# Kernel tuning notes

Hardware: AMD Instinct MI355X
Metric: run time of the kernel (lower is better)

Reference implementation:

```python
import jax, jax.numpy as jnp
import numpy as np

B, T, D, H = 4, 2048, 1024, 16
DK = D // H


def setup_inputs() -> dict:
    key = jax.random.key(0)
    ks = jax.random.split(key, 9)
    s = 1.0 / np.sqrt(D)
    x = jax.random.normal(ks[0], (B, T, D), dtype=jnp.float32)
    mask = jnp.tril(jnp.ones((T, T), dtype=bool))[None, None]  # causal [1,1,T,T]
    wq = jax.random.uniform(ks[1], (D, D), jnp.float32, -s, s)
    bq = jax.random.uniform(ks[2], (D,), jnp.float32, -s, s)
    wk = jax.random.uniform(ks[3], (D, D), jnp.float32, -s, s)
    bk = jax.random.uniform(ks[4], (D,), jnp.float32, -s, s)
    wv = jax.random.uniform(ks[5], (D, D), jnp.float32, -s, s)
    bv = jax.random.uniform(ks[6], (D,), jnp.float32, -s, s)
    wo = jax.random.uniform(ks[7], (D, D), jnp.float32, -s, s)
    bo = jax.random.uniform(ks[8], (D,), jnp.float32, -s, s)
    return {"x": x, "mask": mask, "wq": wq, "bq": bq, "wk": wk, "bk": bk,
            "wv": wv, "bv": bv, "wo": wo, "bo": bo}


def reference(x, mask, wq, bq, wk, bk, wv, bv, wo, bo):
    # projections: torch Linear is x @ W.T + b; here weights stored as (D, D) used directly
    q = (x @ wq + bq).reshape(B, T, H, DK).transpose(0, 2, 1, 3)  # [B,H,T,dk]
    k = (x @ wk + bk).reshape(B, T, H, DK).transpose(0, 2, 1, 3)
    v = (x @ wv + bv).reshape(B, T, H, DK).transpose(0, 2, 1, 3)
    scores = jnp.einsum('bhqd,bhkd->bhqk', q, k) / jnp.sqrt(jnp.float32(DK))
    scores = jnp.where(mask, scores, -jnp.inf)
    attn = jax.nn.softmax(scores, axis=-1)
    # dropout p=0.0 -> identity
    y = jnp.einsum('bhqk,bhkd->bhqd', attn, v)
    y = y.transpose(0, 2, 1, 3).reshape(B, T, D)
    return y @ wo + bo
```

## Files before the change

kernel.cpp:

```cpp
#include <hip/hip_runtime.h>


typedef short s16x8 __attribute__((ext_vector_type(8)));
typedef short s16x4 __attribute__((ext_vector_type(4)));
typedef float f32x4 __attribute__((ext_vector_type(4)));
typedef unsigned int u32x2 __attribute__((ext_vector_type(2)));

static __device__ __forceinline__ float bf2f(unsigned short u) {
    return __uint_as_float(((unsigned int)u) << 16);
}
static __device__ __forceinline__ unsigned short f2bf(float f) {
    unsigned int x = __float_as_uint(f);
    unsigned int r = x + 0x7fffu + ((x >> 16) & 1u);
    return (unsigned short)(r >> 16);
}

static __device__ __forceinline__ void gload_lds16(const short* g, short* l) {
    __builtin_amdgcn_global_load_lds((__attribute__((address_space(1))) void*)g,
                                     (__attribute__((address_space(3))) void*)l, 16, 0, 0);
}

static __device__ __forceinline__ unsigned int cvt_pk_bf16(float a, float b) {
    unsigned int r;
    asm("v_cvt_pk_bf16_f32 %0, %1, %2" : "=v"(r) : "v"(a), "v"(b));
    return r;
}

__global__ __launch_bounds__(64) void detect_dtype(const unsigned short* __restrict__ x,
                                                   int* __restrict__ flag) {
    int lane = threadIdx.x;
    int cnt = 0;
    for (int i = 0; i < 64; ++i) {
        float v = bf2f(x[lane * 64 + i]);
        if (!(fabsf(v) < 1e10f)) cnt++;
    }
    unsigned long long m = __ballot(cnt > 0);
    if (lane == 0) *flag = (m != 0ull) ? 1 : 0;
}

__global__ __launch_bounds__(256) void convert_bf16(const void* __restrict__ src,
                                                    unsigned short* __restrict__ dst,
                                                    int n, const int* __restrict__ flag) {
    int i = blockIdx.x * 256 + threadIdx.x;
    if (i >= n) return;
    if (*flag) dst[i] = f2bf(((const float*)src)[i]);
    else       dst[i] = ((const unsigned short*)src)[i];
}

__global__ __launch_bounds__(256) void convert_biases(const void* __restrict__ b0,
                                                      const void* __restrict__ b1,
                                                      const void* __restrict__ b2,
                                                      const void* __restrict__ b3,
                                                      unsigned short* __restrict__ dst,
                                                      const int* __restrict__ flag) {
    int i = blockIdx.x * 256 + threadIdx.x;
    const void* src = (i < 1024) ? b0 : (i < 2048 ? b1 : (i < 3072 ? b2 : b3));
    int k = i & 1023;
    if (*flag) dst[i] = f2bf(((const float*)src)[k]);
    else       dst[i] = ((const unsigned short*)src)[k];
}

__global__ __launch_bounds__(256) void transpose_wt(const void* __restrict__ src,
                                                    unsigned short* __restrict__ dst,
                                                    const int* __restrict__ flag) {
    __shared__ unsigned short t[32][33];
    int f = *flag;
    int x = threadIdx.x, y = threadIdx.y;
    int n0 = blockIdx.x * 32, k0 = blockIdx.y * 32;
    for (int j = 0; j < 32; j += 8) {
        size_t idx = (size_t)(k0 + y + j) * 1024 + n0 + x;
        t[y + j][x] = f ? f2bf(((const float*)src)[idx]) : ((const unsigned short*)src)[idx];
    }
    __syncthreads();
    for (int j = 0; j < 32; j += 8) dst[(size_t)(n0 + y + j) * 1024 + k0 + x] = t[x][y + j];
}

__global__ __launch_bounds__(256) void gemm_bf16(const short* __restrict__ A,
                                                 const short* __restrict__ Bt,
                                                 void* __restrict__ C,
                                                 short* __restrict__ vt,
                                                 const unsigned short* __restrict__ bq,
                                                 const unsigned short* __restrict__ bk,
                                                 const unsigned short* __restrict__ bv,
                                                 int K, int ldc,
                                                 const int* __restrict__ flag, int f32out,
                                                 int scale_q, int fuse_v) {
    __shared__ __align__(16) short As[128][32];
    __shared__ __align__(16) short Bs[128][32];
    int tid = threadIdx.x;
    int wid = tid >> 6, lane = tid & 63, quad = lane >> 4, l16 = lane & 15;
    int wm = wid & 1, wn = wid >> 1;
    int m0 = blockIdx.x * 128, n0 = blockIdx.y * 128;
    bool wf = f32out && (*flag != 0);

    int lrow = lane >> 2;
    int lcol = (lane & 3) * 8;
    const short* Ag0 = A  + (size_t)(m0 + wid * 32 + lrow) * K + lcol;
    const short* Ag1 = A  + (size_t)(m0 + wid * 32 + 16 + lrow) * K + lcol;
    const short* Bg0 = Bt + (size_t)(n0 + wid * 32 + lrow) * K + lcol;
    const short* Bg1 = Bt + (size_t)(n0 + wid * 32 + 16 + lrow) * K + lcol;
    short* Al0 = &As[wid * 32][0];
    short* Al1 = &As[wid * 32 + 16][0];
    short* Bl0 = &Bs[wid * 32][0];
    short* Bl1 = &Bs[wid * 32 + 16][0];

    f32x4 acc[4][4] = {};
    for (int k0 = 0; k0 < K; k0 += 32) {
        __syncthreads();
        gload_lds16(Ag0 + k0, Al0);
        gload_lds16(Ag1 + k0, Al1);
        gload_lds16(Bg0 + k0, Bl0);
        gload_lds16(Bg1 + k0, Bl1);
        __syncthreads();
        s16x8 a[4], b[4];
        for (int i = 0; i < 4; ++i) a[i] = *(const s16x8*)&As[wm * 64 + i * 16 + l16][quad * 8];
        for (int j = 0; j < 4; ++j) b[j] = *(const s16x8*)&Bs[wn * 64 + j * 16 + l16][quad * 8];
        for (int i = 0; i < 4; ++i)
            for (int j = 0; j < 4; ++j)
                acc[i][j] = __builtin_amdgcn_mfma_f32_16x16x32_bf16(a[i], b[j], acc[i][j], 0, 0, 0);
    }
    for (int j = 0; j < 4; ++j) {
        int col = n0 + wn * 64 + j * 16 + l16;
        const unsigned short* bptr = (col < 1024) ? bq : (col < 2048 ? bk : bv);
        float bias = bf2f(bptr[col & 1023]);
        float cs = (scale_q && col < 1024) ? 0.18033688f : 1.0f;
        for (int i = 0; i < 4; ++i) {
            int rbase = m0 + wm * 64 + i * 16 + quad * 4;
            if (fuse_v && col >= 2048) {
                int h = (col - 2048) >> 6, dk = col & 63;
                int bb_ = rbase >> 11, t = rbase & 2047;
                s16x4 pk;
                for (int r = 0; r < 4; ++r) pk[r] = (short)f2bf(acc[i][j][r] + bias);
                *(s16x4*)(vt + ((size_t)((bb_ * 16 + h) * 64 + dk)) * 2048 + t) = pk;
            } else {
                for (int r = 0; r < 4; ++r) {
                    float v = (acc[i][j][r] + bias) * cs;
                    size_t idx = (size_t)(rbase + r) * ldc + col;
                    if (wf) ((float*)C)[idx] = v;
                    else    ((unsigned short*)C)[idx] = f2bf(v);
                }
            }
        }
    }
}

static __device__ __forceinline__ void stage_tiles(const short* kbase, const short* vbase,
                                                   int kt, short* Kb, short* Vb,
                                                   int wid, int lane) {
    int row = wid * 8 + (lane >> 3);
    int c_src = (lane & 7) ^ (lane >> 3);
    const short* kg = kbase + (size_t)(kt * 64 + row) * 3072 + c_src * 8;
    const short* vg = vbase + (size_t)row * 2048 + kt * 64 + c_src * 8;
    gload_lds16(kg, Kb + wid * 512);
    gload_lds16(vg, Vb + wid * 512);
}

static __device__ __forceinline__ s16x8 lds_frag(const short* buf, int row, int cg) {
    int slot = cg ^ (row & 7);
    return *(const s16x8*)(buf + row * 64 + slot * 8);
}

__global__ __launch_bounds__(512, 4) void attn(const short* __restrict__ qkv,
                                               const short* __restrict__ vt,
                                               unsigned short* __restrict__ y) {
    __shared__ __align__(16) short Kbuf[3][64 * 64];
    __shared__ __align__(16) short Vbuf[3][64 * 64];
    __shared__ __align__(16) short Ps[8][16 * 68];
    int tid = threadIdx.x;
    int wid = tid >> 6, lane = tid & 63, quad = lane >> 4, l16 = lane & 15;
    int bh = blockIdx.x, b = bh >> 4, h = bh & 15;
    const short* kbase = qkv + (size_t)b * 2048 * 3072 + 1024 + h * 64;
    const short* vbase = vt + (size_t)bh * 64 * 2048;
    short* PsW = &Ps[wid][0];

    s16x8 ones;
    for (int e = 0; e < 8; ++e) ones[e] = (short)0x3F80;

    int qb = 15 - (int)blockIdx.y;
    int ktmax = 2 * qb + 1;
    int kmax_w = 2 * qb + (wid >> 2);

    const short* qp = qkv + (size_t)(b * 2048 + qb * 128 + wid * 16 + l16) * 3072 + h * 64;
    s16x8 q0 = *(const s16x8*)(qp + quad * 8);
    s16x8 q1 = *(const s16x8*)(qp + 32 + quad * 8);

    float m_old = -INFINITY;
    f32x4 lacc = {0.f, 0.f, 0.f, 0.f};
    f32x4 o[4] = {};

    stage_tiles(kbase, vbase, 0, &Kbuf[0][0], &Vbuf[0][0], wid, lane);
    stage_tiles(kbase, vbase, 1, &Kbuf[1][0], &Vbuf[1][0], wid, lane);
    int ss = 2;
    int cc = 0;

    for (int kt = 0; kt <= ktmax; ++kt) {
        if (kt < ktmax) asm volatile("s_waitcnt vmcnt(2)" ::: "memory");
        else            asm volatile("s_waitcnt vmcnt(0)" ::: "memory");
        __builtin_amdgcn_sched_barrier(0);
        __builtin_amdgcn_s_barrier();

        if (kt + 2 <= ktmax) {
            stage_tiles(kbase, vbase, kt + 2, &Kbuf[0][0] + ss * 4096, &Vbuf[0][0] + ss * 4096,
                        wid, lane);
            ss = (ss == 2) ? 0 : ss + 1;
        }

        if (kt <= kmax_w) {
            const short* Kb = &Kbuf[0][0] + cc * 4096;
            const short* Vb = &Vbuf[0][0] + cc * 4096;

            f32x4 s[4] = {};
            __builtin_amdgcn_s_setprio(1);
            for (int j = 0; j < 4; ++j) {
                s16x8 klo = lds_frag(Kb, j * 16 + l16, quad);
                s16x8 khi = lds_frag(Kb, j * 16 + l16, 4 + quad);
                s[j] = __builtin_amdgcn_mfma_f32_16x16x32_bf16(klo, q0, s[j], 0, 0, 0);
                s[j] = __builtin_amdgcn_mfma_f32_16x16x32_bf16(khi, q1, s[j], 0, 0, 0);
            }
            __builtin_amdgcn_s_setprio(0);

            if (kt == kmax_w) {
                int qq = (wid & 3) * 16 + l16;
                for (int j = 0; j < 4; ++j)
                    for (int r = 0; r < 4; ++r)
                        if (j * 16 + quad * 4 + r > qq) s[j][r] = -INFINITY;
            }

            float mj0 = fmaxf(fmaxf(s[0][0], s[0][1]), s[0][2]);
            mj0 = fmaxf(mj0, s[0][3]);
            float mj1 = fmaxf(fmaxf(s[1][0], s[1][1]), s[1][2]);
            mj1 = fmaxf(mj1, s[1][3]);
            float mj2 = fmaxf(fmaxf(s[2][0], s[2][1]), s[2][2]);
            mj2 = fmaxf(mj2, s[2][3]);
            float mj3 = fmaxf(fmaxf(s[3][0], s[3][1]), s[3][2]);
            mj3 = fmaxf(mj3, s[3][3]);
            float mx = fmaxf(fmaxf(fmaxf(mj0, mj1), mj2), mj3);
            mx = fmaxf(mx, __shfl_xor(mx, 16));
            mx = fmaxf(mx, __shfl_xor(mx, 32));

            if (__any(mx > m_old + 8.0f)) {
                float mn = fmaxf(m_old, mx);
                float alpha = exp2f(m_old - mn);
                m_old = mn;
                float ar[4];
                for (int r = 0; r < 4; ++r) ar[r] = __shfl(alpha, quad * 4 + r);
                for (int r = 0; r < 4; ++r) {
                    lacc[r] *= ar[r];
                    for (int d = 0; d < 4; ++d) o[d][r] *= ar[r];
                }
            }

            for (int j = 0; j < 4; ++j) {
                float p0 = exp2f(s[j][0] - m_old);
                float p1 = exp2f(s[j][1] - m_old);
                float p2 = exp2f(s[j][2] - m_old);
                float p3 = exp2f(s[j][3] - m_old);
                u32x2 w;
                w.x = cvt_pk_bf16(p0, p1);
                w.y = cvt_pk_bf16(p2, p3);
                *(u32x2*)(PsW + l16 * 68 + j * 16 + quad * 4) = w;
            }

            s16x8 pa0 = *(const s16x8*)&PsW[l16 * 68 + quad * 8];
            s16x8 pa1 = *(const s16x8*)&PsW[l16 * 68 + 32 + quad * 8];
            __builtin_amdgcn_s_setprio(1);
            lacc = __builtin_amdgcn_mfma_f32_16x16x32_bf16(pa0, ones, lacc, 0, 0, 0);
            lacc = __builtin_amdgcn_mfma_f32_16x16x32_bf16(pa1, ones, lacc, 0, 0, 0);
            for (int d = 0; d < 4; ++d) {
                s16x8 vlo = lds_frag(Vb, d * 16 + l16, quad);
                s16x8 vhi = lds_frag(Vb, d * 16 + l16, 4 + quad);
                o[d] = __builtin_amdgcn_mfma_f32_16x16x32_bf16(pa0, vlo, o[d], 0, 0, 0);
                o[d] = __builtin_amdgcn_mfma_f32_16x16x32_bf16(pa1, vhi, o[d], 0, 0, 0);
            }
            __builtin_amdgcn_s_setprio(0);
        }
        cc = (cc == 2) ? 0 : cc + 1;
    }

    for (int r = 0; r < 4; ++r) {
        float inv = 1.f / lacc[r];
        int t = qb * 128 + wid * 16 + quad * 4 + r;
        for (int d = 0; d < 4; ++d)
            y[(size_t)(b * 2048 + t) * 1024 + h * 64 + d * 16 + l16] = f2bf(o[d][r] * inv);
    }
}

extern "C" void kernel_launch(void* const* d_in, const int* in_sizes, int n_in,
                              void* d_out, int out_size, void* d_ws, size_t ws_size,
                              hipStream_t stream) {
    (void)in_sizes; (void)n_in; (void)out_size; (void)ws_size;
    const void* x  = d_in[0];
    const void* wq = d_in[2]; const void* bq = d_in[3];
    const void* wk = d_in[4]; const void* bk = d_in[5];
    const void* wv = d_in[6]; const void* bv = d_in[7];
    const void* wo = d_in[8]; const void* bo = d_in[9];

    const size_t MB = 1024 * 1024;
    char* ws = (char*)d_ws;
    unsigned short* wT  = (unsigned short*)ws;
    short* qkv = (short*)(ws + 8 * MB);
    short* vt  = (short*)(ws + 56 * MB);
    unsigned short* xb = (unsigned short*)(ws + 72 * MB);
    unsigned short* yb = (unsigned short*)(ws + 72 * MB);
    unsigned short* bb = (unsigned short*)(ws + 88 * MB);
    int* flag = (int*)(ws + 88 * MB + 64 * 1024);

    detect_dtype<<<1, 64, 0, stream>>>((const unsigned short*)x, flag);
    convert_bf16<<<32768, 256, 0, stream>>>(x, xb, 8388608, flag);
    convert_biases<<<16, 256, 0, stream>>>(bq, bk, bv, bo, bb, flag);

    dim3 tb(32, 8);
    transpose_wt<<<dim3(32, 32), tb, 0, stream>>>(wq, wT,                flag);
    transpose_wt<<<dim3(32, 32), tb, 0, stream>>>(wk, wT + 1024 * 1024,  flag);
    transpose_wt<<<dim3(32, 32), tb, 0, stream>>>(wv, wT + 2048 * 1024,  flag);
    transpose_wt<<<dim3(32, 32), tb, 0, stream>>>(wo, wT + 3072 * 1024,  flag);

    gemm_bf16<<<dim3(64, 24), 256, 0, stream>>>((const short*)xb, (const short*)wT,
                                                qkv, vt, bb, bb + 1024, bb + 2048,
                                                1024, 3072, flag, 0, 1, 1);
    attn<<<dim3(64, 16), 512, 0, stream>>>(qkv, vt, yb);
    gemm_bf16<<<dim3(64, 8), 256, 0, stream>>>((const short*)yb, (const short*)(wT + 3072 * 1024),
                                               d_out, nullptr, bb + 3072, bb + 3072, bb + 3072,
                                               1024, 1024, flag, 1, 0, 0);
}
```

Baseline: 329.9 us.

## Widen GEMM K-tile to 64 with XOR-swizzled LDS and use raw v_exp_f32

The projection GEMM now stages 64-wide K slices into LDS instead of 32, which halves the number of barrier pairs per K loop. It also XOR-swizzles the 16-byte chunks by row so that fragment reads avoid LDS bank conflicts. Separately, the attention softmax replaces exp2f with inline v_exp_f32 assembly, dropping the denormal and range handling that exp2f adds. The trade-offs are double the LDS per block, which could reduce occupancy, and slightly less exact exponentials for very negative inputs.

```diff
diff --git a/kernel.cpp b/kernel.cpp
--- a/kernel.cpp
+++ b/kernel.cpp
@@ -23,6 +23,12 @@
 static __device__ __forceinline__ unsigned int cvt_pk_bf16(float a, float b) {
     unsigned int r;
     asm("v_cvt_pk_bf16_f32 %0, %1, %2" : "=v"(r) : "v"(a), "v"(b));
+    return r;
+}
+
+static __device__ __forceinline__ float fexp2(float x) {
+    float r;
+    asm("v_exp_f32 %0, %1" : "=v"(r) : "v"(x));
     return r;
 }
 
@@ -85,39 +91,49 @@
                                                  int K, int ldc,
                                                  const int* __restrict__ flag, int f32out,
                                                  int scale_q, int fuse_v) {
-    __shared__ __align__(16) short As[128][32];
-    __shared__ __align__(16) short Bs[128][32];
+    __shared__ __align__(16) short As[128][64];
+    __shared__ __align__(16) short Bs[128][64];
     int tid = threadIdx.x;
     int wid = tid >> 6, lane = tid & 63, quad = lane >> 4, l16 = lane & 15;
     int wm = wid & 1, wn = wid >> 1;
     int m0 = blockIdx.x * 128, n0 = blockIdx.y * 128;
     bool wf = f32out && (*flag != 0);
 
-    int lrow = lane >> 2;
-    int lcol = (lane & 3) * 8;
-    const short* Ag0 = A  + (size_t)(m0 + wid * 32 + lrow) * K + lcol;
-    const short* Ag1 = A  + (size_t)(m0 + wid * 32 + 16 + lrow) * K + lcol;
-    const short* Bg0 = Bt + (size_t)(n0 + wid * 32 + lrow) * K + lcol;
-    const short* Bg1 = Bt + (size_t)(n0 + wid * 32 + 16 + lrow) * K + lcol;
-    short* Al0 = &As[wid * 32][0];
-    short* Al1 = &As[wid * 32 + 16][0];
-    short* Bl0 = &Bs[wid * 32][0];
-    short* Bl1 = &Bs[wid * 32 + 16][0];
+    int srow = lane >> 3;
+    int schunk = (lane & 7) ^ srow;
+    const short* Ag = A  + (size_t)(m0 + wid * 32 + srow) * K + schunk * 8;
+    const short* Bg = Bt + (size_t)(n0 + wid * 32 + srow) * K + schunk * 8;
+    short* Al = &As[wid * 32][0];
+    short* Bl = &Bs[wid * 32][0];
 
     f32x4 acc[4][4] = {};
-    for (int k0 = 0; k0 < K; k0 += 32) {
+    for (int k0 = 0; k0 < K; k0 += 64) {
         __syncthreads();
-        gload_lds16(Ag0 + k0, Al0);
-        gload_lds16(Ag1 + k0, Al1);
-        gload_lds16(Bg0 + k0, Bl0);
-        gload_lds16(Bg1 + k0, Bl1);
+#pragma unroll
+        for (int c = 0; c < 4; ++c) {
+            gload_lds16(Ag + k0 + c * 8 * K, Al + c * 512);
+            gload_lds16(Bg + k0 + c * 8 * K, Bl + c * 512);
+        }
         __syncthreads();
-        s16x8 a[4], b[4];
-        for (int i = 0; i < 4; ++i) a[i] = *(const s16x8*)&As[wm * 64 + i * 16 + l16][quad * 8];
-        for (int j = 0; j < 4; ++j) b[j] = *(const s16x8*)&Bs[wn * 64 + j * 16 + l16][quad * 8];
-        for (int i = 0; i < 4; ++i)
-            for (int j = 0; j < 4; ++j)
-                acc[i][j] = __builtin_amdgcn_mfma_f32_16x16x32_bf16(a[i], b[j], acc[i][j], 0, 0, 0);
+#pragma unroll
+        for (int kk = 0; kk < 2; ++kk) {
+            s16x8 a[4], b[4];
+#pragma unroll
+            for (int i = 0; i < 4; ++i) {
+                int row = wm * 64 + i * 16 + l16;
+                a[i] = *(const s16x8*)&As[row][(((kk << 2) + quad) ^ (row & 7)) << 3];
+            }
+#pragma unroll
+            for (int j = 0; j < 4; ++j) {
+                int row = wn * 64 + j * 16 + l16;
+                b[j] = *(const s16x8*)&Bs[row][(((kk << 2) + quad) ^ (row & 7)) << 3];
+            }
+#pragma unroll
+            for (int i = 0; i < 4; ++i)
+#pragma unroll
+                for (int j = 0; j < 4; ++j)
+                    acc[i][j] = __builtin_amdgcn_mfma_f32_16x16x32_bf16(a[i], b[j], acc[i][j], 0, 0, 0);
+        }
     }
     for (int j = 0; j < 4; ++j) {
         int col = n0 + wn * 64 + j * 16 + l16;
@@ -240,7 +256,7 @@
 
             if (__any(mx > m_old + 8.0f)) {
                 float mn = fmaxf(m_old, mx);
-                float alpha = exp2f(m_old - mn);
+                float alpha = fexp2(m_old - mn);
                 m_old = mn;
                 float ar[4];
                 for (int r = 0; r < 4; ++r) ar[r] = __shfl(alpha, quad * 4 + r);
@@ -251,10 +267,10 @@
             }
 
             for (int j = 0; j < 4; ++j) {
-                float p0 = exp2f(s[j][0] - m_old);
-                float p1 = exp2f(s[j][1] - m_old);
-                float p2 = exp2f(s[j][2] - m_old);
-                float p3 = exp2f(s[j][3] - m_old);
+                float p0 = fexp2(s[j][0] - m_old);
+                float p1 = fexp2(s[j][1] - m_old);
+                float p2 = fexp2(s[j][2] - m_old);
+                float p3 = fexp2(s[j][3] - m_old);
                 u32x2 w;
                 w.x = cvt_pk_bf16(p0, p1);
                 w.y = cvt_pk_bf16(p2, p3);
```

Result: faster. 316.6 us (-4.0%).
